# Kernel optimization log

Measured on AMD Instinct MI355X. Metric: run time of the kernel, lower is better.

Reference implementation:

```python
import jax, jax.numpy as jnp
import numpy as np

B, N, T, D, H = 8, 64, 256, 256, 8
HD = D // H


def _mlp(x, W1, b1, W2, b2):
    # torch nn.Sequential(Linear, GELU(exact), Linear); weights stored pre-transposed
    return jax.nn.gelu(x @ W1 + b1, approximate=False) @ W2 + b2


def setup_inputs() -> dict:
    key = jax.random.key(0)
    ks = jax.random.split(key, 14)
    s = 0.02
    f32 = jnp.float32
    return {
        "padded_batches": jax.random.normal(ks[0], (B, N, T, D), f32),
        "sum_token": jax.random.normal(ks[1], (B, N, 1, D), f32),
        "masks": jax.random.randint(ks[2], (B, N, T), 0, 2).astype(jnp.int32),
        "positions_3d": jax.random.normal(ks[3], (B, N, T, 3), f32),
        "Wq": jax.random.normal(ks[4], (D, D), f32) * s, "bq": jnp.zeros((D,), f32),
        "Wk": jax.random.normal(ks[5], (D, D), f32) * s, "bk": jnp.zeros((D,), f32),
        "Wv": jax.random.normal(ks[6], (D, D), f32) * s, "bv": jnp.zeros((D,), f32),
        "Bw1": jax.random.normal(ks[7], (5, 64), f32) * s, "Bb1": jnp.zeros((64,), f32),
        "Bw2": jax.random.normal(ks[8], (64, H), f32) * s, "Bb2": jnp.zeros((H,), f32),
        "Vw1": jax.random.normal(ks[9], (5, 128), f32) * s, "Vb1": jnp.zeros((128,), f32),
        "Vw2": jax.random.normal(ks[10], (128, D), f32) * s, "Vb2": jnp.zeros((D,), f32),
    }


def reference(padded_batches, sum_token, masks, positions_3d,
              Wq, bq, Wk, bk, Wv, bv,
              Bw1, Bb1, Bw2, Bb2, Vw1, Vb1, Vw2, Vb2):
    Bd, Nd, Td, Dd = padded_batches.shape
    BN = Bd * Nd
    # masked-average summary token (summary_mode='avg'): [B,N,1,D]
    w = masks[..., None].astype(padded_batches.dtype)            # [B,N,T,1]
    denom = jnp.clip(w.sum(-2, keepdims=True), 1e-6)
    summary = (padded_batches * w).sum(-2, keepdims=True) / denom
    # projections (torch Linear: x @ W.T + b; weights here pre-transposed)
    q = (padded_batches @ Wq + bq).reshape(BN, Td, H, HD).transpose(0, 2, 1, 3)  # [BN,H,T,Hd]
    k = (summary @ Wk + bk).reshape(BN, 1, H, HD).transpose(0, 2, 1, 3)          # [BN,H,1,Hd]
    v = (summary @ Wv + bv).reshape(BN, 1, H, HD).transpose(0, 2, 1, 3)
    scale = 1.0 / np.sqrt(HD).astype(np.float32)
    logits = jnp.einsum('bhtd,bhsd->bhts', q, k) * scale          # [BN,H,T,1]
    # relative positional features vs. position summary
    pos_summary = (positions_3d * w).sum(-2, keepdims=True) / denom  # [B,N,1,3]
    diff = positions_3d.reshape(BN, Td, 1, 3) - pos_summary.reshape(BN, 1, 1, 3)  # [BN,T,1,3]
    dist = jnp.linalg.norm(diff, axis=-1, keepdims=True)
    dist2 = (diff ** 2).sum(-1, keepdims=True)
    rel_feat = jnp.concatenate([diff, dist, dist2], axis=-1)      # [BN,T,1,5]
    rel_bias = _mlp(rel_feat, Bw1, Bb1, Bw2, Bb2).transpose(0, 3, 1, 2)  # [BN,H,T,1]
    logits = logits + rel_bias
    neg = jnp.finfo(jnp.float32).min
    attn_mask = jnp.where(masks.reshape(BN, 1, Td, 1) == 0, neg, 0.0)
    logits = logits + attn_mask
    attn_w = jax.nn.softmax(logits, axis=-1)                      # [BN,H,T,1]
    attn = jnp.einsum('bhts,bhsd->bhtd', attn_w, v)               # [BN,H,T,Hd]
    rel_val = _mlp(rel_feat, Vw1, Vb1, Vw2, Vb2)                  # [BN,T,1,D]
    rel_val = rel_val.reshape(BN, Td, 1, H, HD).transpose(0, 3, 1, 2, 4)  # [BN,H,T,1,Hd]
    attn = attn + (attn_w[..., None] * rel_val).sum(-2)
    out = attn.transpose(0, 2, 1, 3).reshape(Bd, Nd, Td, Dd) + padded_batches
    return out
```

## Files before the change

kernel.cpp:

```cpp
#include <hip/hip_runtime.h>
#include <hip/hip_bf16.h>
#include <math.h>


#define BN_TOT 512
#define T_DIM 256
#define D_DIM 256
#define HID 128

typedef __attribute__((ext_vector_type(8))) short short8v;
typedef __attribute__((ext_vector_type(4))) float f32x4;

static __device__ __forceinline__ ushort f2bf(float f) {
    __hip_bfloat16 h = __float2bfloat16(f);
    return *reinterpret_cast<ushort*>(&h);
}

__global__ __launch_bounds__(128) void k_prep(const float* __restrict__ Vw2,
                                              ushort* __restrict__ Vw2t) {
    const int d = blockIdx.x;
    const int k = threadIdx.x;
    Vw2t[d * HID + k] = f2bf(Vw2[k * D_DIM + d]);
}

__global__ __launch_bounds__(512, 1) void k_fused(
    const float* __restrict__ x,
    const int* __restrict__ masks,
    const float* __restrict__ pos,
    const float* __restrict__ Wv,
    const float* __restrict__ bv,
    const float* __restrict__ Vw1,
    const float* __restrict__ Vb1,
    const ushort* __restrict__ Vw2t,
    const float* __restrict__ Vb2,
    float* __restrict__ out)
{
    __shared__ float s_part[8 * 256];
    __shared__ float s_red[4 * 256];
    __shared__ float s_m[256];
    __shared__ float s_sum[256];
    __shared__ float s_vb[256];
    __shared__ float s_rf[256 * 6];
    __shared__ float s_w1[5 * 128];
    __shared__ float s_b1[128];
    __shared__ unsigned char s_hid[T_DIM * HID * 2];

    const int bn  = blockIdx.x;
    const int tid = threadIdx.x;

    const float* xb = x + (size_t)bn * T_DIM * D_DIM;
    const int*   mb = masks + bn * T_DIM;

    if (tid < 256) {
        float m = (float)mb[tid];
        s_m[tid] = m;
        const float* pp = pos + ((size_t)bn * T_DIM + tid) * 3;
        float px = pp[0], py = pp[1], pz = pp[2];
        s_rf[tid * 6 + 0] = px;
        s_rf[tid * 6 + 1] = py;
        s_rf[tid * 6 + 2] = pz;
        s_red[0 * 256 + tid] = m;
        s_red[1 * 256 + tid] = m * px;
        s_red[2 * 256 + tid] = m * py;
        s_red[3 * 256 + tid] = m * pz;
    }
    if (tid < 512) s_w1[tid] = Vw1[tid];
    if (tid < 128) { s_w1[512 + tid] = Vw1[512 + tid]; s_b1[tid] = Vb1[tid]; }
    __syncthreads();

    {
        const int dq = tid & 63, tq = tid >> 6;
        float4 a = make_float4(0.f, 0.f, 0.f, 0.f);
        #pragma unroll 4
        for (int t = tq * 32; t < tq * 32 + 32; ++t) {
            float m = s_m[t];
            float4 xv = *reinterpret_cast<const float4*>(xb + t * D_DIM + dq * 4);
            a.x += m * xv.x; a.y += m * xv.y; a.z += m * xv.z; a.w += m * xv.w;
        }
        *reinterpret_cast<float4*>(s_part + tq * 256 + dq * 4) = a;
    }
    __syncthreads();

    for (int off = 128; off > 0; off >>= 1) {
        if (tid < off) {
            s_red[0 * 256 + tid] += s_red[0 * 256 + tid + off];
            s_red[1 * 256 + tid] += s_red[1 * 256 + tid + off];
            s_red[2 * 256 + tid] += s_red[2 * 256 + tid + off];
            s_red[3 * 256 + tid] += s_red[3 * 256 + tid + off];
        }
        __syncthreads();
    }
    const float inv = 1.0f / fmaxf(s_red[0], 1e-6f);
    const float psx = s_red[1 * 256] * inv;
    const float psy = s_red[2 * 256] * inv;
    const float psz = s_red[3 * 256] * inv;

    if (tid < 256) {
        float s = 0.f;
        #pragma unroll
        for (int q = 0; q < 8; ++q) s += s_part[q * 256 + tid];
        s_sum[tid] = s * inv;
        float dx = s_rf[tid * 6 + 0] - psx;
        float dy = s_rf[tid * 6 + 1] - psy;
        float dz = s_rf[tid * 6 + 2] - psz;
        float d2 = dx * dx + dy * dy + dz * dz;
        s_rf[tid * 6 + 0] = dx; s_rf[tid * 6 + 1] = dy; s_rf[tid * 6 + 2] = dz;
        s_rf[tid * 6 + 3] = sqrtf(d2); s_rf[tid * 6 + 4] = d2;
    }
    __syncthreads();

    {
        const int cg = tid & 15;
        const int c0 = cg * 8;
        float wv[5][8], bb[8];
        #pragma unroll
        for (int e = 0; e < 5; ++e)
            #pragma unroll
            for (int j = 0; j < 8; ++j) wv[e][j] = s_w1[e * 128 + c0 + j];
        #pragma unroll
        for (int j = 0; j < 8; ++j) bb[j] = s_b1[c0 + j];

        #pragma unroll
        for (int s = 0; s < 8; ++s) {
            const int tok = (tid >> 4) + s * 32;
            const float* rf = s_rf + tok * 6;
            const float dx = rf[0], dy = rf[1], dz = rf[2], dd = rf[3], d2 = rf[4];
            uint pk[4];
            #pragma unroll
            for (int jj = 0; jj < 4; ++jj) {
                float g[2];
                #pragma unroll
                for (int h = 0; h < 2; ++h) {
                    const int j = jj * 2 + h;
                    float z = bb[j] + dx * wv[0][j] + dy * wv[1][j] + dz * wv[2][j]
                                    + dd * wv[3][j] + d2 * wv[4][j];
                    g[h] = 0.5f * z * (1.0f + erff(z * 0.70710678118654752f));
                }
                pk[jj] = (uint)f2bf(g[0]) | ((uint)f2bf(g[1]) << 16);
            }
            int byte = tok * 256 + cg * 16;
            byte ^= (tok & 7) << 4;
            *reinterpret_cast<uint4*>(s_hid + byte) = make_uint4(pk[0], pk[1], pk[2], pk[3]);
        }
    }

    {
        const int dq = tid & 63, kq = tid >> 6;
        float4 va = make_float4(0.f, 0.f, 0.f, 0.f);
        #pragma unroll 4
        for (int i = 0; i < 32; ++i) {
            const int k = kq * 32 + i;
            float sc = s_sum[k];
            float4 w = *reinterpret_cast<const float4*>(Wv + k * D_DIM + dq * 4);
            va.x += sc * w.x; va.y += sc * w.y; va.z += sc * w.z; va.w += sc * w.w;
        }
        *reinterpret_cast<float4*>(s_part + kq * 256 + dq * 4) = va;
    }
    __syncthreads();
    if (tid < 256) {
        float r = bv[tid] + Vb2[tid];
        #pragma unroll
        for (int q = 0; q < 8; ++q) r += s_part[q * 256 + tid];
        s_vb[tid] = r;
    }
    __syncthreads();

    const int l  = tid & 63;
    const int wv_id = tid >> 6;
    const int wr = wv_id & 1;
    const int wc = wv_id >> 1;

    f32x4 acc[8][4];
    #pragma unroll
    for (int m = 0; m < 8; ++m)
        #pragma unroll
        for (int n = 0; n < 4; ++n) acc[m][n] = (f32x4){0.f, 0.f, 0.f, 0.f};

    const ushort* bbase = Vw2t + ((size_t)(wc * 64 + (l & 15))) * HID + ((l >> 4) * 8);
    const int col16 = (l >> 4) * 16;

    #pragma unroll
    for (int ks = 0; ks < 4; ++ks) {
        short8v bfr[4];
        #pragma unroll
        for (int n = 0; n < 4; ++n)
            bfr[n] = *reinterpret_cast<const short8v*>(bbase + n * 16 * HID + ks * 32);
        short8v afr[8];
        #pragma unroll
        for (int m = 0; m < 8; ++m) {
            const int tok = wr * 128 + m * 16 + (l & 15);
            int byte = tok * 256 + ks * 64 + col16;
            byte ^= (tok & 7) << 4;
            afr[m] = *reinterpret_cast<const short8v*>(s_hid + byte);
        }
        #pragma unroll
        for (int m = 0; m < 8; ++m)
            #pragma unroll
            for (int n = 0; n < 4; ++n)
                acc[m][n] = __builtin_amdgcn_mfma_f32_16x16x32_bf16(
                    afr[m], bfr[n], acc[m][n], 0, 0, 0);
    }

    #pragma unroll
    for (int m = 0; m < 8; ++m) {
        const int tok = wr * 128 + m * 16 + (l >> 4) * 4;
        const float* xr = xb + (size_t)tok * D_DIM;
        float*       orow = out + ((size_t)bn * T_DIM + tok) * D_DIM;
        #pragma unroll
        for (int n = 0; n < 4; ++n) {
            const int d = wc * 64 + n * 16 + (l & 15);
            const float vb = s_vb[d];
            #pragma unroll
            for (int r = 0; r < 4; ++r) {
                orow[r * D_DIM + d] = xr[r * D_DIM + d] + vb + acc[m][n][r];
            }
        }
    }
}

extern "C" void kernel_launch(void* const* d_in, const int* in_sizes, int n_in,
                              void* d_out, int out_size, void* d_ws, size_t ws_size,
                              hipStream_t stream) {
    const float* x     = (const float*)d_in[0];
    const int*   masks = (const int*)d_in[2];
    const float* pos   = (const float*)d_in[3];
    const float* Wv    = (const float*)d_in[8];
    const float* bv    = (const float*)d_in[9];
    const float* Vw1   = (const float*)d_in[14];
    const float* Vb1   = (const float*)d_in[15];
    const float* Vw2   = (const float*)d_in[16];
    const float* Vb2   = (const float*)d_in[17];
    float* out = (float*)d_out;

    ushort* Vw2t = (ushort*)d_ws;

    k_prep<<<D_DIM, HID, 0, stream>>>(Vw2, Vw2t);
    k_fused<<<BN_TOT, 512, 0, stream>>>(x, masks, pos, Wv, bv,
                                        Vw1, Vb1, Vw2t, Vb2, out);
}
```

Measured before the change: 100.8 us.

## Split fused kernel into summary-reduction and half-sequence main kernels

Splits the single fused kernel into a reduction kernel, which computes the masked summary, the v projection and the position summary into workspace, and a main kernel launched over two halves of T per bn. This doubles the block count and cuts per-block register and LDS use so more blocks can be resident per CU, improving occupancy and latency hiding. The cost is an extra launch, a workspace round-trip, and reading x twice (once in each kernel), which may hit in cache.

```diff
diff --git a/kernel.cpp b/kernel.cpp
--- a/kernel.cpp
+++ b/kernel.cpp
@@ -23,58 +23,43 @@
     Vw2t[d * HID + k] = f2bf(Vw2[k * D_DIM + d]);
 }
 
-__global__ __launch_bounds__(512, 1) void k_fused(
+__global__ __launch_bounds__(256, 8) void k_sum(
     const float* __restrict__ x,
     const int* __restrict__ masks,
     const float* __restrict__ pos,
     const float* __restrict__ Wv,
     const float* __restrict__ bv,
-    const float* __restrict__ Vw1,
-    const float* __restrict__ Vb1,
-    const ushort* __restrict__ Vw2t,
     const float* __restrict__ Vb2,
-    float* __restrict__ out)
+    float* __restrict__ v_ws,
+    float* __restrict__ ps_ws)
 {
-    __shared__ float s_part[8 * 256];
+    __shared__ float s_m[256];
     __shared__ float s_red[4 * 256];
-    __shared__ float s_m[256];
+    __shared__ float s_part[4 * 256];
     __shared__ float s_sum[256];
-    __shared__ float s_vb[256];
-    __shared__ float s_rf[256 * 6];
-    __shared__ float s_w1[5 * 128];
-    __shared__ float s_b1[128];
-    __shared__ unsigned char s_hid[T_DIM * HID * 2];
-
-    const int bn  = blockIdx.x;
-    const int tid = threadIdx.x;
-
+
+    const int bn = blockIdx.x, tid = threadIdx.x;
     const float* xb = x + (size_t)bn * T_DIM * D_DIM;
-    const int*   mb = masks + bn * T_DIM;
-
-    if (tid < 256) {
-        float m = (float)mb[tid];
+
+    {
+        float m = (float)masks[bn * T_DIM + tid];
         s_m[tid] = m;
         const float* pp = pos + ((size_t)bn * T_DIM + tid) * 3;
-        float px = pp[0], py = pp[1], pz = pp[2];
-        s_rf[tid * 6 + 0] = px;
-        s_rf[tid * 6 + 1] = py;
-        s_rf[tid * 6 + 2] = pz;
         s_red[0 * 256 + tid] = m;
-        s_red[1 * 256 + tid] = m * px;
-        s_red[2 * 256 + tid] = m * py;
-        s_red[3 * 256 + tid] = m * pz;
-    }
-    if (tid < 512) s_w1[tid] = Vw1[tid];
-    if (tid < 128) { s_w1[512 + tid] = Vw1[512 + tid]; s_b1[tid] = Vb1[tid]; }
+        s_red[1 * 256 + tid] = m * pp[0];
+        s_red[2 * 256 + tid] = m * pp[1];
+        s_red[3 * 256 + tid] = m * pp[2];
+    }
     __syncthreads();
 
     {
         const int dq = tid & 63, tq = tid >> 6;
         float4 a = make_float4(0.f, 0.f, 0.f, 0.f);
-        #pragma unroll 4
-        for (int t = tq * 32; t < tq * 32 + 32; ++t) {
-            float m = s_m[t];
-            float4 xv = *reinterpret_cast<const float4*>(xb + t * D_DIM + dq * 4);
+        const float* px = xb + (size_t)tq * 64 * D_DIM + dq * 4;
+        #pragma unroll 8
+        for (int i = 0; i < 64; ++i) {
+            float m = s_m[tq * 64 + i];
+            float4 xv = *reinterpret_cast<const float4*>(px + i * D_DIM);
             a.x += m * xv.x; a.y += m * xv.y; a.z += m * xv.z; a.w += m * xv.w;
         }
         *reinterpret_cast<float4*>(s_part + tq * 256 + dq * 4) = a;
@@ -91,18 +76,61 @@
         __syncthreads();
     }
     const float inv = 1.0f / fmaxf(s_red[0], 1e-6f);
-    const float psx = s_red[1 * 256] * inv;
-    const float psy = s_red[2 * 256] * inv;
-    const float psz = s_red[3 * 256] * inv;
-
-    if (tid < 256) {
-        float s = 0.f;
-        #pragma unroll
-        for (int q = 0; q < 8; ++q) s += s_part[q * 256 + tid];
-        s_sum[tid] = s * inv;
-        float dx = s_rf[tid * 6 + 0] - psx;
-        float dy = s_rf[tid * 6 + 1] - psy;
-        float dz = s_rf[tid * 6 + 2] - psz;
+    if (tid < 3) ps_ws[bn * 4 + tid] = s_red[(tid + 1) * 256] * inv;
+
+    s_sum[tid] = (s_part[0 * 256 + tid] + s_part[1 * 256 + tid] +
+                  s_part[2 * 256 + tid] + s_part[3 * 256 + tid]) * inv;
+    __syncthreads();
+
+    {
+        const int dq = tid & 63, kq = tid >> 6;
+        float4 a = make_float4(0.f, 0.f, 0.f, 0.f);
+        #pragma unroll 8
+        for (int i = 0; i < 64; ++i) {
+            const int k = kq * 64 + i;
+            float sc = s_sum[k];
+            float4 w = *reinterpret_cast<const float4*>(Wv + (size_t)k * D_DIM + dq * 4);
+            a.x += sc * w.x; a.y += sc * w.y; a.z += sc * w.z; a.w += sc * w.w;
+        }
+        *reinterpret_cast<float4*>(s_part + kq * 256 + dq * 4) = a;
+    }
+    __syncthreads();
+    v_ws[bn * D_DIM + tid] = s_part[0 * 256 + tid] + s_part[1 * 256 + tid] +
+                             s_part[2 * 256 + tid] + s_part[3 * 256 + tid] +
+                             bv[tid] + Vb2[tid];
+}
+
+__global__ __launch_bounds__(512, 4) void k_main(
+    const float* __restrict__ x,
+    const float* __restrict__ pos,
+    const float* __restrict__ Vw1,
+    const float* __restrict__ Vb1,
+    const ushort* __restrict__ Vw2t,
+    const float* __restrict__ v_ws,
+    const float* __restrict__ ps_ws,
+    float* __restrict__ out)
+{
+    __shared__ float s_rf[128 * 6];
+    __shared__ float s_w1[5 * 128];
+    __shared__ float s_b1[128];
+    __shared__ float s_vb[256];
+    __shared__ unsigned char s_hid[128 * HID * 2];
+
+    const int half = blockIdx.x;
+    const int bn   = blockIdx.y;
+    const int tid  = threadIdx.x;
+    const int t0   = half * 128;
+
+    if (tid < 256) s_vb[tid] = v_ws[bn * D_DIM + tid];
+    for (int i = tid; i < 640; i += 512) s_w1[i] = Vw1[i];
+    if (tid < 128) s_b1[tid] = Vb1[tid];
+
+    const float psx = ps_ws[bn * 4 + 0];
+    const float psy = ps_ws[bn * 4 + 1];
+    const float psz = ps_ws[bn * 4 + 2];
+    if (tid < 128) {
+        const float* pp = pos + ((size_t)bn * T_DIM + t0 + tid) * 3;
+        float dx = pp[0] - psx, dy = pp[1] - psy, dz = pp[2] - psz;
         float d2 = dx * dx + dy * dy + dz * dz;
         s_rf[tid * 6 + 0] = dx; s_rf[tid * 6 + 1] = dy; s_rf[tid * 6 + 2] = dz;
         s_rf[tid * 6 + 3] = sqrtf(d2); s_rf[tid * 6 + 4] = d2;
@@ -116,12 +144,12 @@
         #pragma unroll
         for (int e = 0; e < 5; ++e)
             #pragma unroll
-            for (int j = 0; j < 8; ++j) wv[e][j] = s_w1[e * 128 + c0 + j];
+            for (int j = 0; j < 8; ++j) wv[e][j] = s_w1[e * HID + c0 + j];
         #pragma unroll
         for (int j = 0; j < 8; ++j) bb[j] = s_b1[c0 + j];
 
         #pragma unroll
-        for (int s = 0; s < 8; ++s) {
+        for (int s = 0; s < 4; ++s) {
             const int tok = (tid >> 4) + s * 32;
             const float* rf = s_rf + tok * 6;
             const float dx = rf[0], dy = rf[1], dz = rf[2], dd = rf[3], d2 = rf[4];
@@ -143,36 +171,16 @@
             *reinterpret_cast<uint4*>(s_hid + byte) = make_uint4(pk[0], pk[1], pk[2], pk[3]);
         }
     }
-
-    {
-        const int dq = tid & 63, kq = tid >> 6;
-        float4 va = make_float4(0.f, 0.f, 0.f, 0.f);
-        #pragma unroll 4
-        for (int i = 0; i < 32; ++i) {
-            const int k = kq * 32 + i;
-            float sc = s_sum[k];
-            float4 w = *reinterpret_cast<const float4*>(Wv + k * D_DIM + dq * 4);
-            va.x += sc * w.x; va.y += sc * w.y; va.z += sc * w.z; va.w += sc * w.w;
-        }
-        *reinterpret_cast<float4*>(s_part + kq * 256 + dq * 4) = va;
-    }
-    __syncthreads();
-    if (tid < 256) {
-        float r = bv[tid] + Vb2[tid];
-        #pragma unroll
-        for (int q = 0; q < 8; ++q) r += s_part[q * 256 + tid];
-        s_vb[tid] = r;
-    }
     __syncthreads();
 
     const int l  = tid & 63;
-    const int wv_id = tid >> 6;
-    const int wr = wv_id & 1;
-    const int wc = wv_id >> 1;
-
-    f32x4 acc[8][4];
+    const int wid = tid >> 6;
+    const int wr = wid & 1;
+    const int wc = wid >> 1;
+
+    f32x4 acc[4][4];
     #pragma unroll
-    for (int m = 0; m < 8; ++m)
+    for (int m = 0; m < 4; ++m)
         #pragma unroll
         for (int n = 0; n < 4; ++n) acc[m][n] = (f32x4){0.f, 0.f, 0.f, 0.f};
 
@@ -185,16 +193,16 @@
         #pragma unroll
         for (int n = 0; n < 4; ++n)
             bfr[n] = *reinterpret_cast<const short8v*>(bbase + n * 16 * HID + ks * 32);
-        short8v afr[8];
-        #pragma unroll
-        for (int m = 0; m < 8; ++m) {
-            const int tok = wr * 128 + m * 16 + (l & 15);
+        short8v afr[4];
+        #pragma unroll
+        for (int m = 0; m < 4; ++m) {
+            const int tok = wr * 64 + m * 16 + (l & 15);
             int byte = tok * 256 + ks * 64 + col16;
             byte ^= (tok & 7) << 4;
             afr[m] = *reinterpret_cast<const short8v*>(s_hid + byte);
         }
         #pragma unroll
-        for (int m = 0; m < 8; ++m)
+        for (int m = 0; m < 4; ++m)
             #pragma unroll
             for (int n = 0; n < 4; ++n)
                 acc[m][n] = __builtin_amdgcn_mfma_f32_16x16x32_bf16(
@@ -202,10 +210,10 @@
     }
 
     #pragma unroll
-    for (int m = 0; m < 8; ++m) {
-        const int tok = wr * 128 + m * 16 + (l >> 4) * 4;
-        const float* xr = xb + (size_t)tok * D_DIM;
-        float*       orow = out + ((size_t)bn * T_DIM + tok) * D_DIM;
+    for (int m = 0; m < 4; ++m) {
+        const int tokl = wr * 64 + m * 16 + (l >> 4) * 4;
+        const float* xr   = x   + ((size_t)bn * T_DIM + t0 + tokl) * D_DIM;
+        float*       orow = out + ((size_t)bn * T_DIM + t0 + tokl) * D_DIM;
         #pragma unroll
         for (int n = 0; n < 4; ++n) {
             const int d = wc * 64 + n * 16 + (l & 15);
@@ -233,8 +241,11 @@
     float* out = (float*)d_out;
 
     ushort* Vw2t = (ushort*)d_ws;
+    float*  v_ws = (float*)(Vw2t + D_DIM * HID);
+    float*  ps_ws = v_ws + BN_TOT * D_DIM;
 
     k_prep<<<D_DIM, HID, 0, stream>>>(Vw2, Vw2t);
-    k_fused<<<BN_TOT, 512, 0, stream>>>(x, masks, pos, Wv, bv,
-                                        Vw1, Vb1, Vw2t, Vb2, out);
-}
+    k_sum<<<BN_TOT, 256, 0, stream>>>(x, masks, pos, Wv, bv, Vb2, v_ws, ps_ws);
+    k_main<<<dim3(2, BN_TOT), 512, 0, stream>>>(x, pos, Vw1, Vb1, Vw2t,
+                                                v_ws, ps_ws, out);
+}
```

New measurement: 114.8 us. 1.14x slower.
